# Optimization experiments

Hardware: AMD Instinct MI355X
Metric: run time of the kernel (lower is better)

The kernel has to match this reference:

```python
import jax, jax.numpy as jnp
import numpy as np

EPS_PD = 1e-6    # torch F.pairwise_distance eps (added to x - y before norm)
EPS_NORM = 1e-12  # torch F.normalize eps


def l2_normalize(x):
    n = jnp.sqrt(jnp.sum(x * x, axis=1, keepdims=True))
    return x / jnp.maximum(n, EPS_NORM)


def pairwise_l2(x, y):
    # Faithful to ||x_i - y_j + eps||_2 (torch pairwise_distance adds scalar eps
    # to every coordinate of the difference) but computed via Gram matrices
    D = x.shape[1]
    xx = jnp.sum(x * x, axis=1)            # [B]
    yy = jnp.sum(y * y, axis=1)            # [B]
    xy = x @ y.T                           # [B, B]
    sq = xx[:, None] + yy[None, :] - 2.0 * xy
    # cross terms from the +eps shift: 2*eps*sum(x_i - y_j) + D*eps^2
    sq = sq + 2.0 * EPS_PD * (jnp.sum(x, axis=1)[:, None] - jnp.sum(y, axis=1)[None, :])
    sq = sq + D * (EPS_PD * EPS_PD)
    return jnp.sqrt(jnp.maximum(sq, 0.0))


def setup_inputs() -> dict:
    key = jax.random.key(0)
    k1, k2 = jax.random.split(key)
    B, D = 4096, 512
    low_feature = jax.random.normal(k1, (B, D), dtype=jnp.float32)
    embed_feature = jax.random.normal(k2, (B, D), dtype=jnp.float32)
    id_numpy = jnp.arange(B, dtype=jnp.int64 if jax.config.read('jax_enable_x64') else jnp.int32).reshape(B, 1)
    return {"low_feature": low_feature, "embed_feature": embed_feature, "id_numpy": id_numpy}


def reference(low_feature, embed_feature, id_numpy):
    # ids are unique (arange), so the set()-dedup in the original is identity.
    B = low_feature.shape[0]
    K = B  # k_num == current_batch_size -> x_start = y_start = 0

    low_n = l2_normalize(low_feature)
    emb_n = l2_normalize(embed_feature)

    dist_low = pairwise_l2(low_n, low_n)      # [B, B]
    dist_embed = pairwise_l2(emb_n, emb_n)    # [B, B]

    dl1 = dist_low[: K - 1, : K - 2]
    dl2 = dist_low[: K - 1, 1 : K - 1]
    de1 = dist_embed[: K - 1, : K - 2]
    de2 = dist_embed[: K - 1, 1 : K - 1]

    coeff = jnp.sign(dl1 - dl2) - jnp.sign(de1 - de2)
    dist_embed_inverse = de2 - de1
    loss_structure = jnp.mean(coeff * dist_embed_inverse)
    return loss_structure
```

## Files before the change

kernel.cpp:

```cpp
#include <hip/hip_runtime.h>
#include <hip/hip_bf16.h>
#include <hip/hip_fp8.h>
#include <math.h>

#define BROWS 4096
#define DIM   512
#define YEMB_B 2097152
#define TSTRIDE 191
#define NT 22

typedef float f32x4 __attribute__((ext_vector_type(4)));

__global__ __launch_bounds__(256) void prep4_kernel(
    const float* __restrict__ low, const float* __restrict__ emb,
    unsigned char* __restrict__ Yq,
    float* __restrict__ s_l, float* __restrict__ r_l,
    float* __restrict__ s_e, float* __restrict__ r_e,
    float* __restrict__ out) {
  const int tid = threadIdx.x;
  const int lane = tid & 63, wid = tid >> 6;
  const int rid = blockIdx.x * 4 + wid;
  if (blockIdx.x == 0 && tid == 0) out[0] = 0.f;

  const bool is_low = (rid < BROWS);
  const int row = is_low ? rid : rid - BROWS;
  const float* x = (is_low ? low : emb) + (size_t)row * DIM;

  const float4 v0 = ((const float4*)x)[lane * 2];
  const float4 v1 = ((const float4*)x)[lane * 2 + 1];

  float ss = v0.x * v0.x + v0.y * v0.y + v0.z * v0.z + v0.w * v0.w +
             v1.x * v1.x + v1.y * v1.y + v1.z * v1.z + v1.w * v1.w;
#pragma unroll
  for (int o = 1; o < 64; o <<= 1) ss += __shfl_xor(ss, o, 64);
  const float inv = 1.0f / fmaxf(sqrtf(ss), 1e-12f);

  float y[8] = {v0.x * inv, v0.y * inv, v0.z * inv, v0.w * inv,
                v1.x * inv, v1.y * inv, v1.z * inv, v1.w * inv};

  union { unsigned char b[8]; unsigned long long u; } pk;
  float sv = 0.f, rv = 0.f;
#pragma unroll
  for (int i = 0; i < 8; ++i) {
    pk.b[i] = __hip_fp8_e4m3(y[i]).__x;
    sv += y[i] * y[i];
    rv += y[i];
  }
  ((unsigned long long*)(Yq + (size_t)rid * 512))[lane] = pk.u;

#pragma unroll
  for (int o = 1; o < 64; o <<= 1) {
    sv += __shfl_xor(sv, o, 64);
    rv += __shfl_xor(rv, o, 64);
  }
  if (lane == 0) {
    (is_low ? s_l : s_e)[row] = sv;
    (is_low ? r_l : r_e)[row] = rv;
  }
}

__global__ __launch_bounds__(256, 2) void fused_sym_kernel(
    const unsigned char* __restrict__ Yq,
    const float* __restrict__ s_l, const float* __restrict__ r_l,
    const float* __restrict__ s_e, const float* __restrict__ r_e,
    float* __restrict__ out) {
  __shared__ __align__(16) long lds_l[9728];
  __shared__ float hand_t[3][96][2];
  __shared__ float sred[4];

  const int tri = blockIdx.x >> 1;
  const int half = blockIdx.x & 1;
  int rem = tri, br = 0;
  while (rem >= NT - br) { rem -= NT - br; ++br; }
  const int bc = br + rem;
  const bool diag = (br == bc);
  const bool hasv6 = (half == 0);

  const int tid = threadIdx.x;
  const int lane = tid & 63;
  const int wid = tid >> 6;
  const int wr = wid;
  const int quad = lane >> 4, cpos = lane & 15;
  const int r0 = br * TSTRIDE;
  const int cB = bc * TSTRIDE + half * 96;
  const int tcbase = half * 96;

  int goff[10];
#pragma unroll
  for (int s = 0; s < 10; ++s) {
    const int c = tid + 256 * s;
    const int rp = c >> 3, cc = c & 7;
    int seg, rpl;
    if (rp < 96)       { seg = 0; rpl = rp;       }
    else if (rp < 192) { seg = 1; rpl = rp - 96;  }
    else if (rp < 248) { seg = 2; rpl = rp - 192; }
    else               { seg = 3; rpl = rp - 248; }
    const int rloc = 2 * rpl + (cc >> 2);
    const int gch = (cc & 3) ^ (rpl & 3);
    int base;
    if (seg == 0)      base = min(r0 + rloc, BROWS - 1) * 512;
    else if (seg == 1) base = YEMB_B + min(r0 + rloc, BROWS - 1) * 512;
    else if (seg == 2) base = min(cB + rloc, BROWS - 1) * 512;
    else               base = YEMB_B + min(cB + rloc, BROWS - 1) * 512;
    goff[s] = base + (gch << 4);
  }

  auto STAGE = [&](int t, int b) {
    const int k0 = t * 64;
#pragma unroll
    for (int s = 0; s < 10; ++s) {
      if (s < 9 || tid < 128)
        __builtin_amdgcn_global_load_lds(
            (const __attribute__((address_space(1))) void*)(Yq + goff[s] + k0),
            (__attribute__((address_space(3))) void*)(
                ((char*)lds_l) + b * 38912 + (tid + 256 * s) * 16),
            16, 0, 0);
    }
  };

  const int RaH = (48 * wr + cpos) >> 1;
  const int s3a = RaH & 3;
  const int aoff = RaH * 128 + (cpos & 1) * 64 + (quad & 1) * 8;
  const int s3b = (cpos >> 1) & 3;
  const int boff = (cpos >> 1) * 128 + (cpos & 1) * 64 + (quad & 1) * 8;
  const int iaL = aoff >> 3;
  const int iaE = (12288 + aoff) >> 3;
  const int ibL = (24576 + boff) >> 3;
  const int ibE = (31744 + boff) >> 3;

  f32x4 accl[3][7], acce[3][7];
#pragma unroll
  for (int u = 0; u < 3; ++u)
#pragma unroll
    for (int v = 0; v < 7; ++v) {
      accl[u][v] = (f32x4)(0.f);
      acce[u][v] = (f32x4)(0.f);
    }

  STAGE(0, 0);

  for (int t = 0; t < 8; ++t) {
    if (t < 7) STAGE(t + 1, (t + 1) & 1);
    if (t == 7)      asm volatile("s_waitcnt vmcnt(0)" ::: "memory");
    else if (wid < 2) asm volatile("s_waitcnt vmcnt(10)" ::: "memory");
    else             asm volatile("s_waitcnt vmcnt(9)" ::: "memory");
    __builtin_amdgcn_s_barrier();
    __builtin_amdgcn_sched_barrier(0);

    const int bo = (t & 1) * 4864;
#pragma unroll
    for (int kk = 0; kk < 2; ++kk) {
      const int q = 2 * kk + (quad >> 1);
      const int qa2 = ((q ^ s3a) << 1);
      const int qb2 = ((q ^ s3b) << 1);
      {
        long a[3], b[7];
#pragma unroll
        for (int u = 0; u < 3; ++u) a[u] = lds_l[bo + iaL + qa2 + u * 128];
#pragma unroll
        for (int v = 0; v < 6; ++v) b[v] = lds_l[bo + ibL + qb2 + v * 128];
        if (hasv6) b[6] = lds_l[bo + ibL + qb2 + 768];
        __builtin_amdgcn_s_setprio(1);
#pragma unroll
        for (int u = 0; u < 3; ++u)
#pragma unroll
          for (int v = 0; v < 6; ++v)
            accl[u][v] = __builtin_amdgcn_mfma_f32_16x16x32_fp8_fp8(
                a[u], b[v], accl[u][v], 0, 0, 0);
        if (hasv6) {
#pragma unroll
          for (int u = 0; u < 3; ++u)
            accl[u][6] = __builtin_amdgcn_mfma_f32_16x16x32_fp8_fp8(
                a[u], b[6], accl[u][6], 0, 0, 0);
        }
        __builtin_amdgcn_s_setprio(0);
      }
      {
        long a[3], b[7];
#pragma unroll
        for (int u = 0; u < 3; ++u) a[u] = lds_l[bo + iaE + qa2 + u * 128];
#pragma unroll
        for (int v = 0; v < 6; ++v) b[v] = lds_l[bo + ibE + qb2 + v * 128];
        if (hasv6) b[6] = lds_l[bo + ibE + qb2 + 768];
        __builtin_amdgcn_s_setprio(1);
#pragma unroll
        for (int u = 0; u < 3; ++u)
#pragma unroll
          for (int v = 0; v < 6; ++v)
            acce[u][v] = __builtin_amdgcn_mfma_f32_16x16x32_fp8_fp8(
                a[u], b[v], acce[u][v], 0, 0, 0);
        if (hasv6) {
#pragma unroll
          for (int u = 0; u < 3; ++u)
            acce[u][6] = __builtin_amdgcn_mfma_f32_16x16x32_fp8_fp8(
                a[u], b[6], acce[u][6], 0, 0, 0);
        }
        __builtin_amdgcn_s_setprio(0);
      }
    }
    __builtin_amdgcn_sched_barrier(0);
    __builtin_amdgcn_s_barrier();
    __builtin_amdgcn_sched_barrier(0);
  }

  const float epst = (float)DIM * 1e-6f * 1e-6f;
#pragma unroll
  for (int v = 0; v < 7; ++v) {
    const int j = min(cB + 16 * v + cpos, BROWS - 1);
    const float sjl = s_l[j], rjl = r_l[j];
    const float sje = s_e[j], rje = r_e[j];
#pragma unroll
    for (int u = 0; u < 3; ++u)
#pragma unroll
      for (int r = 0; r < 4; ++r) {
        const int i = min(r0 + 48 * wr + 16 * u + 4 * quad + r, BROWS - 1);
        const float sql = s_l[i] + sjl - 2.f * accl[u][v][r] +
                          2e-6f * (r_l[i] - rjl) + epst;
        accl[u][v][r] = sqrtf(fmaxf(sql, 0.f));
        const float sqe = s_e[i] + sje - 2.f * acce[u][v][r] +
                          2e-6f * (r_e[i] - rje) + epst;
        acce[u][v][r] = sqrtf(fmaxf(sqe, 0.f));
      }
  }

  if (quad == 0 && wr >= 1) {
#pragma unroll
    for (int v = 0; v < 6; ++v) {
      hand_t[wr - 1][16 * v + cpos][0] = accl[0][v][0];
      hand_t[wr - 1][16 * v + cpos][1] = acce[0][v][0];
    }
  }
  __syncthreads();

  float sum = 0.f;

  const int srcin = (lane & 48) | ((cpos + 1) & 15);
#pragma unroll
  for (int u = 0; u < 3; ++u)
#pragma unroll
    for (int r = 0; r < 4; ++r) {
      const int trow = 48 * wr + 16 * u + 4 * quad + r;
      const int i = r0 + trow;
      const bool rowok = (trow <= TSTRIDE - 1) && (i <= BROWS - 2);
#pragma unroll
      for (int v = 0; v < 6; ++v) {
        const float dl1 = accl[u][v][r], de1 = acce[u][v][r];
        float dl2 = __shfl(dl1, srcin, 64);
        float de2 = __shfl(de1, srcin, 64);
        const float dlb = __shfl(accl[u][v + 1][r], lane & 48, 64);
        const float deb = __shfl(acce[u][v + 1][r], lane & 48, 64);
        if (cpos == 15) { dl2 = dlb; de2 = deb; }
        const int tc = tcbase + 16 * v + cpos;
        const int j = cB + 16 * v + cpos;
        if (rowok && tc <= TSTRIDE - 1 && j <= BROWS - 3) {
          const float aa = dl1 - dl2, bb = de1 - de2;
          const float coeff = (float)((aa > 0.f) - (aa < 0.f)) -
                              (float)((bb > 0.f) - (bb < 0.f));
          sum += coeff * (de2 - de1);
        }
      }
    }

  if (!diag) {
#pragma unroll
    for (int u = 0; u < 3; ++u)
#pragma unroll
      for (int v = 0; v < 6; ++v) {
        const int tc = tcbase + 16 * v + cpos;
        const int ii = cB + 16 * v + cpos;
        const bool colok = (tc <= TSTRIDE - 1) && (ii <= BROWS - 2);
#pragma unroll
        for (int r = 0; r < 4; ++r) {
          const int trow = 48 * wr + 16 * u + 4 * quad + r;
          const int jj = r0 + trow;
          float dl2, de2;
          if (r < 3) {
            dl2 = accl[u][v][r + 1];
            de2 = acce[u][v][r + 1];
          } else {
            const float dlq = __shfl(accl[u][v][0], (lane + 16) & 63, 64);
            const float deq = __shfl(acce[u][v][0], (lane + 16) & 63, 64);
            const int un = (u < 2) ? u + 1 : u;
            const float dlu = __shfl(accl[un][v][0], cpos, 64);
            const float deu = __shfl(acce[un][v][0], cpos, 64);
            if (quad < 3)    { dl2 = dlq; de2 = deq; }
            else if (u < 2)  { dl2 = dlu; de2 = deu; }
            else             { dl2 = hand_t[wr][16 * v + cpos][0];
                               de2 = hand_t[wr][16 * v + cpos][1]; }
          }
          if (colok && trow <= TSTRIDE - 1 && jj <= BROWS - 3) {
            const float dl1 = accl[u][v][r], de1 = acce[u][v][r];
            const float aa = dl1 - dl2, bb = de1 - de2;
            const float coeff = (float)((aa > 0.f) - (aa < 0.f)) -
                                (float)((bb > 0.f) - (bb < 0.f));
            sum += coeff * (de2 - de1);
          }
        }
      }
  }

#pragma unroll
  for (int o = 32; o; o >>= 1) sum += __shfl_down(sum, o, 64);
  if (lane == 0) sred[wid] = sum;
  __syncthreads();
  if (tid == 0) {
    const float scale = 1.0f / ((float)(BROWS - 1) * (float)(BROWS - 2));
    float t = 0.f;
#pragma unroll
    for (int w = 0; w < 4; ++w) t += sred[w];
    atomicAdd(out, t * scale);
  }
}

extern "C" void kernel_launch(void* const* d_in, const int* in_sizes, int n_in,
                              void* d_out, int out_size, void* d_ws,
                              size_t ws_size, hipStream_t stream) {
  const float* low = (const float*)d_in[0];
  const float* emb = (const float*)d_in[1];
  float* out = (float*)d_out;

  unsigned char* Yq = (unsigned char*)d_ws;
  float* s_l = (float*)(Yq + 2 * (size_t)BROWS * DIM);
  float* r_l = s_l + BROWS;
  float* s_e = r_l + BROWS;
  float* r_e = s_e + BROWS;

  prep4_kernel<<<2 * BROWS / 4, 256, 0, stream>>>(low, emb, Yq, s_l, r_l, s_e, r_e, out);
  fused_sym_kernel<<<NT * (NT + 1), 256, 0, stream>>>(Yq, s_l, r_l, s_e, r_e, out);
}
```

Baseline: 110.5 us.

## Drop symmetric triangle tiling; use full tile grid with transposed MFMA and algebraic epilogue

Replaces the upper-triangular tile schedule, which evaluated both the direct and transposed loss terms per tile, with a full NT×NT grid in which each tile handles only the direct term. Operands are swapped so accumulator rows run along the column index, and adjacent-column differences become in-register neighbours. The epilogue skips the sqrt for the low-feature distances. Because sqrt is monotone, the sign of dl1-dl2 is taken from the Gram difference plus precomputed per-column norm terms staged in shared memory. The loss term is rewritten as |x| plus a signed x, and the hasv6 half-tile specialisation is dropped. The cost is roughly double the MFMA work and tile loads (full grid instead of a triangle), traded for a much lighter epilogue and fewer shuffles.

Measured after the change: 119.8 us. 8.5% more time.

```diff
diff --git a/kernel.cpp b/kernel.cpp
--- a/kernel.cpp
+++ b/kernel.cpp
@@ -65,16 +65,15 @@
     const float* __restrict__ s_e, const float* __restrict__ r_e,
     float* __restrict__ out) {
   __shared__ __align__(16) long lds_l[9728];
-  __shared__ float hand_t[3][96][2];
+  __shared__ __align__(16) float aE[192];
+  __shared__ __align__(16) float bE[120];
+  __shared__ __align__(16) float cL[120];
   __shared__ float sred[4];
 
-  const int tri = blockIdx.x >> 1;
+  const int b2 = blockIdx.x >> 1;
   const int half = blockIdx.x & 1;
-  int rem = tri, br = 0;
-  while (rem >= NT - br) { rem -= NT - br; ++br; }
-  const int bc = br + rem;
-  const bool diag = (br == bc);
-  const bool hasv6 = (half == 0);
+  const int br = b2 / NT;
+  const int bc = b2 % NT;
 
   const int tid = threadIdx.x;
   const int lane = tid & 63;
@@ -84,6 +83,18 @@
   const int r0 = br * TSTRIDE;
   const int cB = bc * TSTRIDE + half * 96;
   const int tcbase = half * 96;
+  const float epst = (float)DIM * 1e-6f * 1e-6f;
+
+  if (tid < 192) {
+    const int gi = min(r0 + tid, BROWS - 1);
+    aE[tid] = s_e[gi] + 2e-6f * r_e[gi] + epst;
+  }
+  if (tid < 116) {
+    const int gj = min(cB + tid, BROWS - 1);
+    const int gj1 = min(cB + tid + 1, BROWS - 1);
+    bE[tid] = s_e[gj] - 2e-6f * r_e[gj];
+    cL[tid] = (s_l[gj] - s_l[gj1]) - 2e-6f * (r_l[gj] - r_l[gj1]);
+  }
 
   int goff[10];
 #pragma unroll
@@ -128,22 +139,22 @@
   const int ibL = (24576 + boff) >> 3;
   const int ibE = (31744 + boff) >> 3;
 
-  f32x4 accl[3][7], acce[3][7];
-#pragma unroll
-  for (int u = 0; u < 3; ++u)
-#pragma unroll
-    for (int v = 0; v < 7; ++v) {
-      accl[u][v] = (f32x4)(0.f);
-      acce[u][v] = (f32x4)(0.f);
+  f32x4 accl[7][3], acce[7][3];
+#pragma unroll
+  for (int jb = 0; jb < 7; ++jb)
+#pragma unroll
+    for (int ib = 0; ib < 3; ++ib) {
+      accl[jb][ib] = (f32x4)(0.f);
+      acce[jb][ib] = (f32x4)(0.f);
     }
 
   STAGE(0, 0);
 
   for (int t = 0; t < 8; ++t) {
     if (t < 7) STAGE(t + 1, (t + 1) & 1);
-    if (t == 7)      asm volatile("s_waitcnt vmcnt(0)" ::: "memory");
+    if (t == 7)       asm volatile("s_waitcnt vmcnt(0)" ::: "memory");
     else if (wid < 2) asm volatile("s_waitcnt vmcnt(10)" ::: "memory");
-    else             asm volatile("s_waitcnt vmcnt(9)" ::: "memory");
+    else              asm volatile("s_waitcnt vmcnt(9)" ::: "memory");
     __builtin_amdgcn_s_barrier();
     __builtin_amdgcn_sched_barrier(0);
 
@@ -154,47 +165,33 @@
       const int qa2 = ((q ^ s3a) << 1);
       const int qb2 = ((q ^ s3b) << 1);
       {
-        long a[3], b[7];
-#pragma unroll
-        for (int u = 0; u < 3; ++u) a[u] = lds_l[bo + iaL + qa2 + u * 128];
-#pragma unroll
-        for (int v = 0; v < 6; ++v) b[v] = lds_l[bo + ibL + qb2 + v * 128];
-        if (hasv6) b[6] = lds_l[bo + ibL + qb2 + 768];
+        long a[7], b[3];
+#pragma unroll
+        for (int jb = 0; jb < 7; ++jb) a[jb] = lds_l[bo + ibL + qb2 + jb * 128];
+#pragma unroll
+        for (int ib = 0; ib < 3; ++ib) b[ib] = lds_l[bo + iaL + qa2 + ib * 128];
         __builtin_amdgcn_s_setprio(1);
 #pragma unroll
-        for (int u = 0; u < 3; ++u)
-#pragma unroll
-          for (int v = 0; v < 6; ++v)
-            accl[u][v] = __builtin_amdgcn_mfma_f32_16x16x32_fp8_fp8(
-                a[u], b[v], accl[u][v], 0, 0, 0);
-        if (hasv6) {
-#pragma unroll
-          for (int u = 0; u < 3; ++u)
-            accl[u][6] = __builtin_amdgcn_mfma_f32_16x16x32_fp8_fp8(
-                a[u], b[6], accl[u][6], 0, 0, 0);
-        }
+        for (int jb = 0; jb < 7; ++jb)
+#pragma unroll
+          for (int ib = 0; ib < 3; ++ib)
+            accl[jb][ib] = __builtin_amdgcn_mfma_f32_16x16x32_fp8_fp8(
+                a[jb], b[ib], accl[jb][ib], 0, 0, 0);
         __builtin_amdgcn_s_setprio(0);
       }
       {
-        long a[3], b[7];
-#pragma unroll
-        for (int u = 0; u < 3; ++u) a[u] = lds_l[bo + iaE + qa2 + u * 128];
-#pragma unroll
-        for (int v = 0; v < 6; ++v) b[v] = lds_l[bo + ibE + qb2 + v * 128];
-        if (hasv6) b[6] = lds_l[bo + ibE + qb2 + 768];
+        long a[7], b[3];
+#pragma unroll
+        for (int jb = 0; jb < 7; ++jb) a[jb] = lds_l[bo + ibE + qb2 + jb * 128];
+#pragma unroll
+        for (int ib = 0; ib < 3; ++ib) b[ib] = lds_l[bo + iaE + qa2 + ib * 128];
         __builtin_amdgcn_s_setprio(1);
 #pragma unroll
-        for (int u = 0; u < 3; ++u)
-#pragma unroll
-          for (int v = 0; v < 6; ++v)
-            acce[u][v] = __builtin_amdgcn_mfma_f32_16x16x32_fp8_fp8(
-                a[u], b[v], acce[u][v], 0, 0, 0);
-        if (hasv6) {
-#pragma unroll
-          for (int u = 0; u < 3; ++u)
-            acce[u][6] = __builtin_amdgcn_mfma_f32_16x16x32_fp8_fp8(
-                a[u], b[6], acce[u][6], 0, 0, 0);
-        }
+        for (int jb = 0; jb < 7; ++jb)
+#pragma unroll
+          for (int ib = 0; ib < 3; ++ib)
+            acce[jb][ib] = __builtin_amdgcn_mfma_f32_16x16x32_fp8_fp8(
+                a[jb], b[ib], acce[jb][ib], 0, 0, 0);
         __builtin_amdgcn_s_setprio(0);
       }
     }
@@ -203,100 +200,58 @@
     __builtin_amdgcn_sched_barrier(0);
   }
 
-  const float epst = (float)DIM * 1e-6f * 1e-6f;
-#pragma unroll
-  for (int v = 0; v < 7; ++v) {
-    const int j = min(cB + 16 * v + cpos, BROWS - 1);
-    const float sjl = s_l[j], rjl = r_l[j];
-    const float sje = s_e[j], rje = r_e[j];
-#pragma unroll
-    for (int u = 0; u < 3; ++u)
+  float sum = 0.f;
+
+#pragma unroll
+  for (int ib = 0; ib < 3; ++ib) {
+    const int irow = 48 * wr + 16 * ib + cpos;
+    const int gi = r0 + irow;
+    const bool rowok = (irow <= TSTRIDE - 1) && (gi <= BROWS - 2);
+    const float ai = aE[irow];
+
+    float deJ[4], glJ[4];
+    {
+      const float4 bj = ((const float4*)bE)[quad];
 #pragma unroll
       for (int r = 0; r < 4; ++r) {
-        const int i = min(r0 + 48 * wr + 16 * u + 4 * quad + r, BROWS - 1);
-        const float sql = s_l[i] + sjl - 2.f * accl[u][v][r] +
-                          2e-6f * (r_l[i] - rjl) + epst;
-        accl[u][v][r] = sqrtf(fmaxf(sql, 0.f));
-        const float sqe = s_e[i] + sje - 2.f * acce[u][v][r] +
-                          2e-6f * (r_e[i] - rje) + epst;
-        acce[u][v][r] = sqrtf(fmaxf(sqe, 0.f));
-      }
-  }
-
-  if (quad == 0 && wr >= 1) {
-#pragma unroll
-    for (int v = 0; v < 6; ++v) {
-      hand_t[wr - 1][16 * v + cpos][0] = accl[0][v][0];
-      hand_t[wr - 1][16 * v + cpos][1] = acce[0][v][0];
-    }
-  }
-  __syncthreads();
-
-  float sum = 0.f;
-
-  const int srcin = (lane & 48) | ((cpos + 1) & 15);
-#pragma unroll
-  for (int u = 0; u < 3; ++u)
-#pragma unroll
-    for (int r = 0; r < 4; ++r) {
-      const int trow = 48 * wr + 16 * u + 4 * quad + r;
-      const int i = r0 + trow;
-      const bool rowok = (trow <= TSTRIDE - 1) && (i <= BROWS - 2);
-#pragma unroll
-      for (int v = 0; v < 6; ++v) {
-        const float dl1 = accl[u][v][r], de1 = acce[u][v][r];
-        float dl2 = __shfl(dl1, srcin, 64);
-        float de2 = __shfl(de1, srcin, 64);
-        const float dlb = __shfl(accl[u][v + 1][r], lane & 48, 64);
-        const float deb = __shfl(acce[u][v + 1][r], lane & 48, 64);
-        if (cpos == 15) { dl2 = dlb; de2 = deb; }
-        const int tc = tcbase + 16 * v + cpos;
-        const int j = cB + 16 * v + cpos;
-        if (rowok && tc <= TSTRIDE - 1 && j <= BROWS - 3) {
-          const float aa = dl1 - dl2, bb = de1 - de2;
-          const float coeff = (float)((aa > 0.f) - (aa < 0.f)) -
-                              (float)((bb > 0.f) - (bb < 0.f));
-          sum += coeff * (de2 - de1);
-        }
-      }
-    }
-
-  if (!diag) {
-#pragma unroll
-    for (int u = 0; u < 3; ++u)
-#pragma unroll
-      for (int v = 0; v < 6; ++v) {
-        const int tc = tcbase + 16 * v + cpos;
-        const int ii = cB + 16 * v + cpos;
-        const bool colok = (tc <= TSTRIDE - 1) && (ii <= BROWS - 2);
-#pragma unroll
-        for (int r = 0; r < 4; ++r) {
-          const int trow = 48 * wr + 16 * u + 4 * quad + r;
-          const int jj = r0 + trow;
-          float dl2, de2;
-          if (r < 3) {
-            dl2 = accl[u][v][r + 1];
-            de2 = acce[u][v][r + 1];
-          } else {
-            const float dlq = __shfl(accl[u][v][0], (lane + 16) & 63, 64);
-            const float deq = __shfl(acce[u][v][0], (lane + 16) & 63, 64);
-            const int un = (u < 2) ? u + 1 : u;
-            const float dlu = __shfl(accl[un][v][0], cpos, 64);
-            const float deu = __shfl(acce[un][v][0], cpos, 64);
-            if (quad < 3)    { dl2 = dlq; de2 = deq; }
-            else if (u < 2)  { dl2 = dlu; de2 = deu; }
-            else             { dl2 = hand_t[wr][16 * v + cpos][0];
-                               de2 = hand_t[wr][16 * v + cpos][1]; }
-          }
-          if (colok && trow <= TSTRIDE - 1 && jj <= BROWS - 3) {
-            const float dl1 = accl[u][v][r], de1 = acce[u][v][r];
-            const float aa = dl1 - dl2, bb = de1 - de2;
-            const float coeff = (float)((aa > 0.f) - (aa < 0.f)) -
-                                (float)((bb > 0.f) - (bb < 0.f));
-            sum += coeff * (de2 - de1);
-          }
-        }
-      }
+        deJ[r] = sqrtf(fmaxf(ai + bj[r] - 2.f * acce[0][ib][r], 0.f));
+        glJ[r] = accl[0][ib][r];
+      }
+    }
+
+#pragma unroll
+    for (int jb = 0; jb < 6; ++jb) {
+      const float4 bn = ((const float4*)bE)[4 * (jb + 1) + quad];
+      float deN[4], glN[4];
+#pragma unroll
+      for (int r = 0; r < 4; ++r) {
+        deN[r] = sqrtf(fmaxf(ai + bn[r] - 2.f * acce[jb + 1][ib][r], 0.f));
+        glN[r] = accl[jb + 1][ib][r];
+      }
+      const float deq = __shfl(deJ[0], (lane + 16) & 63, 64);
+      const float dec = __shfl(deN[0], lane & 15, 64);
+      const float glq = __shfl(glJ[0], (lane + 16) & 63, 64);
+      const float glc = __shfl(glN[0], lane & 15, 64);
+      const float de2r3 = (quad < 3) ? deq : dec;
+      const float gl2r3 = (quad < 3) ? glq : glc;
+
+      const float4 cl = ((const float4*)cL)[4 * jb + quad];
+#pragma unroll
+      for (int r = 0; r < 4; ++r) {
+        const float de1 = deJ[r];
+        const float de2 = (r < 3) ? deJ[r + 1] : de2r3;
+        const float g2 = (r < 3) ? glJ[r + 1] : gl2r3;
+        const float x = de2 - de1;
+        const float Dl = cl[r] - 2.f * (glJ[r] - g2);
+        const float tterm = fabsf(x) +
+                            (Dl > 0.f ? x : (Dl < 0.f ? -x : 0.f));
+        const int jcol = tcbase + 16 * jb + 4 * quad + r;
+        const int gj = cB + 16 * jb + 4 * quad + r;
+        if (rowok && jcol <= TSTRIDE - 1 && gj <= BROWS - 3) sum += tterm;
+      }
+#pragma unroll
+      for (int r = 0; r < 4; ++r) { deJ[r] = deN[r]; glJ[r] = glN[r]; }
+    }
   }
 
 #pragma unroll
@@ -326,5 +281,5 @@
   float* r_e = s_e + BROWS;
 
   prep4_kernel<<<2 * BROWS / 4, 256, 0, stream>>>(low, emb, Yq, s_l, r_l, s_e, r_e, out);
-  fused_sym_kernel<<<NT * (NT + 1), 256, 0, stream>>>(Yq, s_l, r_l, s_e, r_e, out);
+  fused_sym_kernel<<<NT * NT * 2, 256, 0, stream>>>(Yq, s_l, r_l, s_e, r_e, out);
 }
```
